# Optimization experiments

Hardware: AMD Instinct MI355X
Metric: run time of the kernel (lower is better)

## Reference

```python
import jax, jax.numpy as jnp
import numpy as np

N, M_NODES, E_EDGES, D = 32, 128, 256, 128  # note: D must equal M_NODES (see original convK1 constraint)


def setup_inputs() -> dict:
    key = jax.random.key(0)
    k1, k2, k3, k4, k5 = jax.random.split(key, 5)
    feature_matrix = jax.random.normal(k1, (N, M_NODES, D), dtype=jnp.float32)
    incidence_matrix = (jax.random.uniform(k2, (N, M_NODES, E_EDGES)) < 0.25).astype(jnp.float32)
    # grouped Conv1d(m, m*m, d, groups=m) weights reshaped to (m, m, d); bias (m, m)
    Wkk = jax.random.normal(k3, (M_NODES, M_NODES, D), dtype=jnp.float32) * (1.0 / np.sqrt(D))
    bkk = jax.random.normal(k4, (M_NODES, M_NODES), dtype=jnp.float32) * 0.01
    # Conv1d(m, 1, 1) weights: (1, m, 1) -> vector of length m (== d)
    w1 = jax.random.normal(k5, (D,), dtype=jnp.float32) * (1.0 / np.sqrt(D))
    b1 = jnp.zeros((), dtype=jnp.float32)
    return {"feature_matrix": feature_matrix, "incidence_matrix": incidence_matrix,
            "Wkk": Wkk, "bkk": bkk, "w1": w1, "b1": b1}


def reference(feature_matrix, incidence_matrix, Wkk, bkk, w1, b1):
    n, m, d = feature_matrix.shape
    e = incidence_matrix.shape[-1]
    # incidence broadcast: (N,m,1,d) * (N,m,e,1) -> (N,m,e,d) -> (N,e,m,d) -> (N*e, m, d)
    region = feature_matrix[:, :, None, :] * incidence_matrix[:, :, :, None]
    region = region.transpose(0, 2, 1, 3).reshape(n * e, m, d)
    # grouped conv with full-length kernel == per-row dot products
    logits = jnp.einsum('bid,ijd->bij', region, Wkk) + bkk  # (B, m, m)
    multiplier = jax.nn.softmax(logits, axis=-1)
    transformed = jax.nn.relu(jnp.einsum('bij,bjd->bid', multiplier, region))  # (B, m, d)
    # Conv1d(m,1,1) on (B, d, m): weighted sum over the feature axis (valid since d == m)
    pooled = jnp.einsum('bld,d->bl', transformed, w1) + b1  # (B, m) with m == d
    return pooled.reshape(n, e, d)
```

## Files before the change

### kernel.cpp

```cpp
#include <hip/hip_runtime.h>

#define NN 32
#define MM 128
#define EE 256
#define DD 128
#define ELB 16

typedef __attribute__((ext_vector_type(8))) short short8;
typedef __attribute__((ext_vector_type(4))) float f32x4;

union U16x8 { uint4 u; short8 s; };

static __device__ __forceinline__ unsigned short f2bf(float f) {
  union { float f; unsigned u; } v; v.f = f;
  unsigned r = v.u + 0x7FFFu + ((v.u >> 16) & 1u);
  return (unsigned short)(r >> 16);
}

__global__ __launch_bounds__(128, 1)
void k_prep(const float* __restrict__ X, const float* __restrict__ Wkk,
            const float* __restrict__ bkk,
            unsigned short* __restrict__ P1g, unsigned short* __restrict__ P0g) {
  const int i  = blockIdx.x;
  const int ty = threadIdx.x >> 6;
  const int l  = threadIdx.x & 63;
  const int lr = l & 15, lg = l >> 4;

  short8 a[4];
  {
    const int n = ty * 16 + lr;
    const float* xp = X + (n * MM + i) * DD + lg * 8;
#pragma unroll
    for (int k = 0; k < 4; ++k) {
      float4 v0 = *(const float4*)(xp + k * 32);
      float4 v1 = *(const float4*)(xp + k * 32 + 4);
      short8 s;
      s[0]=(short)f2bf(v0.x); s[1]=(short)f2bf(v0.y); s[2]=(short)f2bf(v0.z); s[3]=(short)f2bf(v0.w);
      s[4]=(short)f2bf(v1.x); s[5]=(short)f2bf(v1.y); s[6]=(short)f2bf(v1.z); s[7]=(short)f2bf(v1.w);
      a[k] = s;
    }
  }
  f32x4 acc[8];
#pragma unroll
  for (int cf = 0; cf < 8; ++cf) acc[cf] = (f32x4){0.f, 0.f, 0.f, 0.f};

#pragma unroll
  for (int k = 0; k < 4; ++k) {
#pragma unroll
    for (int cf = 0; cf < 8; ++cf) {
      const int j = cf * 16 + lr;
      const float* wp = Wkk + (i * MM + j) * DD + k * 32 + lg * 8;
      float4 v0 = *(const float4*)(wp);
      float4 v1 = *(const float4*)(wp + 4);
      short8 b;
      b[0]=(short)f2bf(v0.x); b[1]=(short)f2bf(v0.y); b[2]=(short)f2bf(v0.z); b[3]=(short)f2bf(v0.w);
      b[4]=(short)f2bf(v1.x); b[5]=(short)f2bf(v1.y); b[6]=(short)f2bf(v1.z); b[7]=(short)f2bf(v1.w);
      acc[cf] = __builtin_amdgcn_mfma_f32_16x16x32_bf16(a[k], b, acc[cf], 0, 0, 0);
    }
  }

  float bk[8];
#pragma unroll
  for (int cf = 0; cf < 8; ++cf) bk[cf] = bkk[i * MM + cf * 16 + lr];

#pragma unroll
  for (int r = 0; r < 4; ++r) {
    float v[8], m = -1e30f;
#pragma unroll
    for (int cf = 0; cf < 8; ++cf) { v[cf] = acc[cf][r] + bk[cf]; m = fmaxf(m, v[cf]); }
#pragma unroll
    for (int s = 1; s < 16; s <<= 1) m = fmaxf(m, __shfl_xor(m, s, 64));
    float sum = 0.f;
#pragma unroll
    for (int cf = 0; cf < 8; ++cf) { v[cf] = __expf(v[cf] - m); sum += v[cf]; }
#pragma unroll
    for (int s = 1; s < 16; s <<= 1) sum += __shfl_xor(sum, s, 64);
    const float inv = 1.f / sum;
    const int n = ty * 16 + lg * 4 + r;
    unsigned short* dst = P1g + (n * MM + i) * MM;
#pragma unroll
    for (int cf = 0; cf < 8; ++cf) dst[cf * 16 + lr] = f2bf(v[cf] * inv);
  }

  if (ty == 0) {
    float v0 = bkk[i * MM + l], v1 = bkk[i * MM + 64 + l];
    float m = fmaxf(v0, v1);
#pragma unroll
    for (int s = 1; s < 64; s <<= 1) m = fmaxf(m, __shfl_xor(m, s, 64));
    v0 = __expf(v0 - m); v1 = __expf(v1 - m);
    float sum = v0 + v1;
#pragma unroll
    for (int s = 1; s < 64; s <<= 1) sum += __shfl_xor(sum, s, 64);
    const float inv = 1.f / sum;
    P0g[i * MM + l]      = f2bf(v0 * inv);
    P0g[i * MM + 64 + l] = f2bf(v1 * inv);
  }
}

__global__ __launch_bounds__(256, 1)
void k_xt(const float* __restrict__ X, unsigned short* __restrict__ XTg) {
  __shared__ float xs[128][129];
  const int n = blockIdx.x, t = threadIdx.x;
#pragma unroll
  for (int it = 0; it < 16; ++it) {
    int idx = it * 256 + t;
    int j = idx >> 5, dq = idx & 31;
    float4 v = *(const float4*)(X + (n * MM + j) * DD + dq * 4);
    xs[j][dq * 4 + 0] = v.x; xs[j][dq * 4 + 1] = v.y;
    xs[j][dq * 4 + 2] = v.z; xs[j][dq * 4 + 3] = v.w;
  }
  __syncthreads();
  const int d = t >> 1, jh = t & 1;
  unsigned* dst = (unsigned*)XTg + (n * DD + d) * (MM / 2) + jh * 32;
#pragma unroll
  for (int jj = 0; jj < 32; ++jj) {
    int j = jh * 64 + jj * 2;
    unsigned u0 = f2bf(xs[j][d]), u1 = f2bf(xs[j + 1][d]);
    dst[jj] = u0 | (u1 << 16);
  }
}

__global__ __launch_bounds__(256, 2)
void k_main(const unsigned short* __restrict__ P0g, const unsigned short* __restrict__ P1g,
            const unsigned short* __restrict__ XTg, const float* __restrict__ inc,
            const float* __restrict__ w1, const float* __restrict__ b1p,
            float* __restrict__ out) {
  __shared__ alignas(128) unsigned short Plds[2][128][128];
  __shared__ unsigned int bitm[ELB][4];
  __shared__ alignas(16) unsigned short mrow[ELB][128];

  const int n  = blockIdx.x & 31;
  const int eg = blockIdx.x >> 5;
  const int t  = threadIdx.x;
  const int w  = t >> 6, l = t & 63, lr = l & 15, lg = l >> 4;

  {
    char* d0 = (char*)&Plds[0][0][0];
    char* d1 = (char*)&Plds[1][0][0];
    const uint4* s0 = (const uint4*)P0g;
    const uint4* s1 = (const uint4*)(P1g + n * MM * MM);
#pragma unroll
    for (int it = 0; it < 8; ++it) {
      int idx = it * 256 + t;
      int off = (idx * 16) ^ (((idx >> 4) & 7) << 4);
      *(uint4*)(d0 + off) = s0[idx];
      *(uint4*)(d1 + off) = s1[idx];
    }
  }
  if (t < ELB * 4) {
    int el = t >> 2, wd = t & 3;
    int e = eg * ELB + el;
    unsigned bm = 0;
    for (int b = 0; b < 32; ++b) {
      float v = inc[(n * MM + wd * 32 + b) * EE + e];
      if (v != 0.f) bm |= (1u << b);
    }
    bitm[el][wd] = bm;
  }

  short8 B[8][4];
  {
    const unsigned short* xb = XTg + n * DD * MM;
#pragma unroll
    for (int cf = 0; cf < 8; ++cf) {
      int drow = cf * 16 + lr;
#pragma unroll
      for (int k = 0; k < 4; ++k) {
        U16x8 tmp; tmp.u = *(const uint4*)(xb + drow * MM + k * 32 + lg * 8);
        B[cf][k] = tmp.s;
      }
    }
  }
  float wv[8];
#pragma unroll
  for (int cf = 0; cf < 8; ++cf) wv[cf] = w1[cf * 16 + lr];
  const float b1v = b1p[0];
  __syncthreads();

  if (t < ELB * 8) {
    int el = t >> 3, j0 = (t & 7) * 16;
    unsigned wd = bitm[el][j0 >> 5];
    int sh = j0 & 31;
    unsigned short* mp = &mrow[el][j0];
#pragma unroll
    for (int b = 0; b < 16; ++b) mp[b] = ((wd >> (sh + b)) & 1u) ? 0xFFFFu : 0u;
  }
  __syncthreads();

  const char* pbase = (const char*)&Plds[0][0][0];
  float* outp = out + (n * EE + eg * ELB) * MM;

#pragma unroll 1
  for (int el = 0; el < ELB; ++el) {
    const unsigned selw = bitm[el][w];
    f32x4 acc[2][8];
#pragma unroll
    for (int rf = 0; rf < 2; ++rf)
#pragma unroll
      for (int cf = 0; cf < 8; ++cf) acc[rf][cf] = (f32x4){0.f, 0.f, 0.f, 0.f};

#pragma unroll
    for (int k = 0; k < 4; ++k) {
      uint4 mm = *(const uint4*)((const char*)&mrow[el][0] + k * 64 + lg * 16);
#pragma unroll
      for (int rf = 0; rf < 2; ++rf) {
        const int row = w * 32 + rf * 16 + lr;
        const unsigned sel = (selw >> (rf * 16 + lr)) & 1u;
        const int off = (row * 256 + k * 64 + lg * 16) ^ ((row & 7) << 4);
        U16x8 av; av.u = *(const uint4*)(pbase + sel * 32768u + off);
        av.u.x &= mm.x; av.u.y &= mm.y; av.u.z &= mm.z; av.u.w &= mm.w;
#pragma unroll
        for (int cf = 0; cf < 8; ++cf)
          acc[rf][cf] = __builtin_amdgcn_mfma_f32_16x16x32_bf16(av.s, B[cf][k], acc[rf][cf], 0, 0, 0);
      }
    }
    float p[2][4];
#pragma unroll
    for (int rf = 0; rf < 2; ++rf)
#pragma unroll
      for (int r = 0; r < 4; ++r) {
        float sum = 0.f;
#pragma unroll
        for (int cf = 0; cf < 8; ++cf) sum += fmaxf(acc[rf][cf][r], 0.f) * wv[cf];
        p[rf][r] = sum;
      }
#pragma unroll
    for (int s = 1; s < 16; s <<= 1)
#pragma unroll
      for (int rf = 0; rf < 2; ++rf)
#pragma unroll
        for (int r = 0; r < 4; ++r) p[rf][r] += __shfl_xor(p[rf][r], s, 64);
    if (lr == 0) {
#pragma unroll
      for (int rf = 0; rf < 2; ++rf) {
        float* op = outp + el * MM + w * 32 + rf * 16 + lg * 4;
#pragma unroll
        for (int r = 0; r < 4; ++r) op[r] = p[rf][r] + b1v;
      }
    }
  }
}

extern "C" void kernel_launch(void* const* d_in, const int* in_sizes, int n_in,
                              void* d_out, int out_size, void* d_ws, size_t ws_size,
                              hipStream_t stream) {
  const float* X   = (const float*)d_in[0];
  const float* inc = (const float*)d_in[1];
  const float* Wkk = (const float*)d_in[2];
  const float* bkk = (const float*)d_in[3];
  const float* w1  = (const float*)d_in[4];
  const float* b1  = (const float*)d_in[5];
  float* out = (float*)d_out;

  unsigned short* P1g = (unsigned short*)d_ws;
  unsigned short* XTg = P1g + NN * MM * DD;
  unsigned short* P0g = XTg + NN * MM * DD;

  hipLaunchKernelGGL(k_prep, dim3(128), dim3(128), 0, stream, X, Wkk, bkk, P1g, P0g);
  hipLaunchKernelGGL(k_xt,   dim3(32),  dim3(256), 0, stream, X, XTg);
  hipLaunchKernelGGL(k_main, dim3(512), dim3(256), 0, stream, P0g, P1g, XTg, inc, w1, b1, out);
}
```

Baseline: 57.87 us.

## Hold softmax rows in registers, split rows across blocks, pool via MFMA

Measured after the change: 62.41 us. +7.9%, slower.

```diff
diff --git a/kernel.cpp b/kernel.cpp
--- a/kernel.cpp
+++ b/kernel.cpp
@@ -120,61 +120,76 @@
   }
 }
 
+__global__ __launch_bounds__(256, 1)
+void k_binc(const float* __restrict__ inc, unsigned* __restrict__ bmap) {
+  const int n = blockIdx.x, e = threadIdx.x;
+  unsigned bm0 = 0, bm1 = 0, bm2 = 0, bm3 = 0;
+#pragma unroll 4
+  for (int j = 0; j < 32; ++j)
+    if (inc[(n * MM + j) * EE + e] != 0.f) bm0 |= 1u << j;
+#pragma unroll 4
+  for (int j = 0; j < 32; ++j)
+    if (inc[(n * MM + 32 + j) * EE + e] != 0.f) bm1 |= 1u << j;
+#pragma unroll 4
+  for (int j = 0; j < 32; ++j)
+    if (inc[(n * MM + 64 + j) * EE + e] != 0.f) bm2 |= 1u << j;
+#pragma unroll 4
+  for (int j = 0; j < 32; ++j)
+    if (inc[(n * MM + 96 + j) * EE + e] != 0.f) bm3 |= 1u << j;
+  uint4 v; v.x = bm0; v.y = bm1; v.z = bm2; v.w = bm3;
+  *(uint4*)(bmap + (n * EE + e) * 4) = v;
+}
+
 __global__ __launch_bounds__(256, 2)
 void k_main(const unsigned short* __restrict__ P0g, const unsigned short* __restrict__ P1g,
-            const unsigned short* __restrict__ XTg, const float* __restrict__ inc,
+            const unsigned short* __restrict__ XTg, const unsigned* __restrict__ bmap,
             const float* __restrict__ w1, const float* __restrict__ b1p,
             float* __restrict__ out) {
-  __shared__ alignas(128) unsigned short Plds[2][128][128];
-  __shared__ unsigned int bitm[ELB][4];
+  __shared__ unsigned bitm[ELB][4];
   __shared__ alignas(16) unsigned short mrow[ELB][128];
 
-  const int n  = blockIdx.x & 31;
-  const int eg = blockIdx.x >> 5;
-  const int t  = threadIdx.x;
-  const int w  = t >> 6, l = t & 63, lr = l & 15, lg = l >> 4;
-
+  const int bid = blockIdx.x;
+  const int n = bid & 31, eg = (bid >> 5) & 15, rh = bid >> 9;
+  const int t = threadIdx.x, w = t >> 6, l = t & 63, lr = l & 15, lg = l >> 4;
+  const int i_lane = rh * 64 + w * 16 + lr;
+
+  if (t < ELB)
+    *(uint4*)&bitm[t][0] = *(const uint4*)(bmap + (n * EE + eg * ELB + t) * 4);
+
+  uint4 p0[4], p1[4];
   {
-    char* d0 = (char*)&Plds[0][0][0];
-    char* d1 = (char*)&Plds[1][0][0];
-    const uint4* s0 = (const uint4*)P0g;
-    const uint4* s1 = (const uint4*)(P1g + n * MM * MM);
-#pragma unroll
-    for (int it = 0; it < 8; ++it) {
-      int idx = it * 256 + t;
-      int off = (idx * 16) ^ (((idx >> 4) & 7) << 4);
-      *(uint4*)(d0 + off) = s0[idx];
-      *(uint4*)(d1 + off) = s1[idx];
-    }
-  }
-  if (t < ELB * 4) {
-    int el = t >> 2, wd = t & 3;
-    int e = eg * ELB + el;
-    unsigned bm = 0;
-    for (int b = 0; b < 32; ++b) {
-      float v = inc[(n * MM + wd * 32 + b) * EE + e];
-      if (v != 0.f) bm |= (1u << b);
-    }
-    bitm[el][wd] = bm;
-  }
-
-  short8 B[8][4];
+    const unsigned short* pb0 = P0g + i_lane * MM;
+    const unsigned short* pb1 = P1g + n * MM * MM + i_lane * MM;
+#pragma unroll
+    for (int k = 0; k < 4; ++k) {
+      p0[k] = *(const uint4*)(pb0 + k * 32 + lg * 8);
+      p1[k] = *(const uint4*)(pb1 + k * 32 + lg * 8);
+    }
+  }
+  short8 x[8][4];
   {
     const unsigned short* xb = XTg + n * DD * MM;
 #pragma unroll
-    for (int cf = 0; cf < 8; ++cf) {
-      int drow = cf * 16 + lr;
+    for (int cf = 0; cf < 8; ++cf)
 #pragma unroll
       for (int k = 0; k < 4; ++k) {
-        U16x8 tmp; tmp.u = *(const uint4*)(xb + drow * MM + k * 32 + lg * 8);
-        B[cf][k] = tmp.s;
+        U16x8 tmp; tmp.u = *(const uint4*)(xb + (cf * 16 + lr) * MM + k * 32 + lg * 8);
+        x[cf][k] = tmp.s;
       }
-    }
-  }
-  float wv[8];
-#pragma unroll
-  for (int cf = 0; cf < 8; ++cf) wv[cf] = w1[cf * 16 + lr];
+  }
+  short8 w1pk[4];
+#pragma unroll
+  for (int p = 0; p < 4; ++p) {
+    float4 a = *(const float4*)(w1 + (2 * p) * 16 + lg * 4);
+    float4 b = *(const float4*)(w1 + (2 * p + 1) * 16 + lg * 4);
+    short8 s;
+    s[0]=(short)f2bf(a.x); s[1]=(short)f2bf(a.y); s[2]=(short)f2bf(a.z); s[3]=(short)f2bf(a.w);
+    s[4]=(short)f2bf(b.x); s[5]=(short)f2bf(b.y); s[6]=(short)f2bf(b.z); s[7]=(short)f2bf(b.w);
+    w1pk[p] = s;
+  }
   const float b1v = b1p[0];
+  const int selsh = (w & 1) * 16 + lr;
+  const int selwd = rh * 2 + (w >> 1);
   __syncthreads();
 
   if (t < ELB * 8) {
@@ -187,57 +202,52 @@
   }
   __syncthreads();
 
-  const char* pbase = (const char*)&Plds[0][0][0];
-  float* outp = out + (n * EE + eg * ELB) * MM;
+  float* outp = out + (n * EE + eg * ELB) * MM + rh * 64 + w * 16 + lg * 4;
 
 #pragma unroll 1
   for (int el = 0; el < ELB; ++el) {
-    const unsigned selw = bitm[el][w];
-    f32x4 acc[2][8];
-#pragma unroll
-    for (int rf = 0; rf < 2; ++rf)
-#pragma unroll
-      for (int cf = 0; cf < 8; ++cf) acc[rf][cf] = (f32x4){0.f, 0.f, 0.f, 0.f};
+    const unsigned selw = bitm[el][selwd];
+    const bool sel = ((selw >> selsh) & 1u) != 0u;
+    f32x4 acc[8];
+#pragma unroll
+    for (int cf = 0; cf < 8; ++cf) acc[cf] = (f32x4){0.f, 0.f, 0.f, 0.f};
 
 #pragma unroll
     for (int k = 0; k < 4; ++k) {
       uint4 mm = *(const uint4*)((const char*)&mrow[el][0] + k * 64 + lg * 16);
-#pragma unroll
-      for (int rf = 0; rf < 2; ++rf) {
-        const int row = w * 32 + rf * 16 + lr;
-        const unsigned sel = (selw >> (rf * 16 + lr)) & 1u;
-        const int off = (row * 256 + k * 64 + lg * 16) ^ ((row & 7) << 4);
-        U16x8 av; av.u = *(const uint4*)(pbase + sel * 32768u + off);
-        av.u.x &= mm.x; av.u.y &= mm.y; av.u.z &= mm.z; av.u.w &= mm.w;
-#pragma unroll
-        for (int cf = 0; cf < 8; ++cf)
-          acc[rf][cf] = __builtin_amdgcn_mfma_f32_16x16x32_bf16(av.s, B[cf][k], acc[rf][cf], 0, 0, 0);
-      }
-    }
-    float p[2][4];
-#pragma unroll
-    for (int rf = 0; rf < 2; ++rf)
-#pragma unroll
-      for (int r = 0; r < 4; ++r) {
-        float sum = 0.f;
-#pragma unroll
-        for (int cf = 0; cf < 8; ++cf) sum += fmaxf(acc[rf][cf][r], 0.f) * wv[cf];
-        p[rf][r] = sum;
-      }
-#pragma unroll
-    for (int s = 1; s < 16; s <<= 1)
-#pragma unroll
-      for (int rf = 0; rf < 2; ++rf)
-#pragma unroll
-        for (int r = 0; r < 4; ++r) p[rf][r] += __shfl_xor(p[rf][r], s, 64);
-    if (lr == 0) {
-#pragma unroll
-      for (int rf = 0; rf < 2; ++rf) {
-        float* op = outp + el * MM + w * 32 + rf * 16 + lg * 4;
-#pragma unroll
-        for (int r = 0; r < 4; ++r) op[r] = p[rf][r] + b1v;
-      }
-    }
+      U16x8 pvv;
+      pvv.u.x = (sel ? p1[k].x : p0[k].x) & mm.x;
+      pvv.u.y = (sel ? p1[k].y : p0[k].y) & mm.y;
+      pvv.u.z = (sel ? p1[k].z : p0[k].z) & mm.z;
+      pvv.u.w = (sel ? p1[k].w : p0[k].w) & mm.w;
+#pragma unroll
+      for (int cf = 0; cf < 8; ++cf)
+        acc[cf] = __builtin_amdgcn_mfma_f32_16x16x32_bf16(x[cf][k], pvv.s, acc[cf], 0, 0, 0);
+    }
+
+    f32x4 acc3a = (f32x4){b1v, b1v, b1v, b1v};
+    f32x4 acc3b = (f32x4){0.f, 0.f, 0.f, 0.f};
+#pragma unroll
+    for (int p = 0; p < 4; ++p) {
+      float a0 = fmaxf(acc[2*p][0], 0.f), a1 = fmaxf(acc[2*p][1], 0.f);
+      float a2 = fmaxf(acc[2*p][2], 0.f), a3 = fmaxf(acc[2*p][3], 0.f);
+      float c0 = fmaxf(acc[2*p+1][0], 0.f), c1 = fmaxf(acc[2*p+1][1], 0.f);
+      float c2 = fmaxf(acc[2*p+1][2], 0.f), c3 = fmaxf(acc[2*p+1][3], 0.f);
+      unsigned u0, u1, u2, u3;
+      asm("v_cvt_pk_bf16_f32 %0, %1, %2" : "=v"(u0) : "v"(a0), "v"(a1));
+      asm("v_cvt_pk_bf16_f32 %0, %1, %2" : "=v"(u1) : "v"(a2), "v"(a3));
+      asm("v_cvt_pk_bf16_f32 %0, %1, %2" : "=v"(u2) : "v"(c0), "v"(c1));
+      asm("v_cvt_pk_bf16_f32 %0, %1, %2" : "=v"(u3) : "v"(c2), "v"(c3));
+      U16x8 uu; uu.u.x = u0; uu.u.y = u1; uu.u.z = u2; uu.u.w = u3;
+      if (p & 1)
+        acc3b = __builtin_amdgcn_mfma_f32_16x16x32_bf16(uu.s, w1pk[p], acc3b, 0, 0, 0);
+      else
+        acc3a = __builtin_amdgcn_mfma_f32_16x16x32_bf16(uu.s, w1pk[p], acc3a, 0, 0, 0);
+    }
+    acc3a[0] += acc3b[0]; acc3a[1] += acc3b[1];
+    acc3a[2] += acc3b[2]; acc3a[3] += acc3b[3];
+
+    if (lr == 0) *(float4*)(outp + el * MM) = *(float4*)&acc3a;
   }
 }
 
@@ -255,8 +265,10 @@
   unsigned short* P1g = (unsigned short*)d_ws;
   unsigned short* XTg = P1g + NN * MM * DD;
   unsigned short* P0g = XTg + NN * MM * DD;
+  unsigned* bmap = (unsigned*)(P0g + MM * MM);
 
   hipLaunchKernelGGL(k_prep, dim3(128), dim3(128), 0, stream, X, Wkk, bkk, P1g, P0g);
   hipLaunchKernelGGL(k_xt,   dim3(32),  dim3(256), 0, stream, X, XTg);
-  hipLaunchKernelGGL(k_main, dim3(512), dim3(256), 0, stream, P0g, P1g, XTg, inc, w1, b1, out);
-}
+  hipLaunchKernelGGL(k_binc, dim3(32),  dim3(256), 0, stream, inc, bmap);
+  hipLaunchKernelGGL(k_main, dim3(1024), dim3(256), 0, stream, P0g, P1g, XTg, bmap, w1, b1, out);
+}
```
